# Performance work log

Measured on AMD Instinct MI355X. Metric: run time of the kernel, lower is better.

Reference implementation:

```python
import jax, jax.numpy as jnp
import numpy as np

E = 8        # moe_num_experts
TOPK = 2     # moe_topk
H = 1024     # hidden_size
I = 1024     # intermediate_size
ISH = I * 2  # shared experts intermediate (intermediate_size * moe_num_shared_experts)
B, S = 2, 1024


def setup_inputs() -> dict:
    key = jax.random.key(0)
    ks = jax.random.split(key, 7)
    s = 0.02
    return {
        "hidden_states": jax.random.normal(ks[0], (B, S, H), jnp.float32),
        "w_router": jax.random.normal(ks[1], (H, E), jnp.float32) * s,
        "fc1_w": jax.random.normal(ks[2], (E, H, 2 * I), jnp.float32) * s,
        "fc2_w": jax.random.normal(ks[3], (E, I, H), jnp.float32) * s,
        "gate_w": jax.random.normal(ks[4], (H, ISH), jnp.float32) * s,
        "up_w": jax.random.normal(ks[5], (H, ISH), jnp.float32) * s,
        "down_w": jax.random.normal(ks[6], (ISH, H), jnp.float32) * s,
    }


def reference(hidden_states, w_router, fc1_w, fc2_w, gate_w, up_w, down_w):
    orig_shape = hidden_states.shape
    x = hidden_states.reshape(-1, orig_shape[-1])  # [N, H]

    # --- router: top-k + softmax over the top-k logits ---
    logits = x @ w_router                               # [N, E]
    top_logits, top_idx = jax.lax.top_k(logits, TOPK)   # [N, K]
    scores = jax.nn.softmax(top_logits, axis=-1)        # [N, K]

    # --- permute tokens so same-expert tokens are contiguous ---
    flat_idx = top_idx.reshape(-1)                      # [N*K]
    sorted_idx = jnp.argsort(flat_idx)                  # [N*K]
    permuted = x[sorted_idx // TOPK]                    # [N*K, H]
    eid = flat_idx[sorted_idx]                          # expert id per permuted slot

    # --- grouped expert SwiGLU MLP (masked per-expert GEMMs; masked rows
    #     contribute exactly zero since silu(0)*0 = 0 and 0 @ W = 0) ---
    out_perm = jnp.zeros((permuted.shape[0], orig_shape[-1]), x.dtype)
    for e in range(E):
        m = (eid == e).astype(x.dtype)[:, None]         # [N*K, 1]
        h1 = (permuted * m) @ fc1_w[e]                  # [N*K, 2I]
        proj, gate = jnp.split(h1, 2, axis=-1)
        out_perm = out_perm + (jax.nn.silu(proj) * gate) @ fc2_w[e]

    # --- unpermute and combine with router scores ---
    unperm = jnp.zeros_like(out_perm).at[sorted_idx].set(out_perm)  # [N*K, H]
    moe_out = (unperm.reshape(-1, TOPK, orig_shape[-1]) * scores[:, :, None]).sum(axis=1)
    moe_out = moe_out.reshape(orig_shape)

    # --- shared experts (LlamaMLP, SwiGLU) ---
    shared = (jax.nn.silu(hidden_states @ gate_w) * (hidden_states @ up_w)) @ down_w
    return moe_out + shared
```

## Files before the change

### kernel.cpp

```cpp
#include <hip/hip_runtime.h>
#include <cstdint>


#define E_ 8
#define H_ 1024
#define I_ 1024
#define ISH_ 2048
#define NTOK 2048

typedef unsigned short u16;
using bf16x8 = __attribute__((ext_vector_type(8))) __bf16;
using f32x4  = __attribute__((ext_vector_type(4))) float;

__device__ __forceinline__ u16 f2bf(float f) {
  union { float f; unsigned u; } v; v.f = f;
  unsigned r = v.u + 0x7fffu + ((v.u >> 16) & 1u);
  return (u16)(r >> 16);
}
__device__ __forceinline__ float bf2f(u16 u) {
  union { unsigned u; float f; } v; v.u = ((unsigned)u) << 16; return v.f;
}
__device__ __forceinline__ unsigned pk2(float lo, float hi) {
  return ((unsigned)f2bf(hi) << 16) | (unsigned)f2bf(lo);
}

typedef __attribute__((address_space(1))) const void glb_v;
typedef __attribute__((address_space(3))) void lds_v;
__device__ __forceinline__ void gl16(const void* g, void* l) {
  __builtin_amdgcn_global_load_lds((glb_v*)g, (lds_v*)l, 16, 0, 0);
}

__device__ __forceinline__ void router_body(const float* __restrict__ x,
                                            const float* __restrict__ wr,
                                            float* __restrict__ scores,
                                            int* __restrict__ cnt,
                                            int* __restrict__ list, int tk) {
  int lane = threadIdx.x & 63;
  const float* xr = x + (size_t)tk * H_;
  float acc[E_];
#pragma unroll
  for (int e = 0; e < E_; ++e) acc[e] = 0.f;
  int h0 = lane * 16;
#pragma unroll 4
  for (int i = 0; i < 16; ++i) {
    float xv = xr[h0 + i];
    const float* w = wr + (size_t)(h0 + i) * E_;
#pragma unroll
    for (int e = 0; e < E_; ++e) acc[e] = fmaf(xv, w[e], acc[e]);
  }
#pragma unroll
  for (int off = 32; off > 0; off >>= 1) {
#pragma unroll
    for (int e = 0; e < E_; ++e) acc[e] += __shfl_xor(acc[e], off, 64);
  }
  if (lane == 0) {
    int e0 = 0; float m0 = acc[0];
#pragma unroll
    for (int e = 1; e < E_; ++e) if (acc[e] > m0) { m0 = acc[e]; e0 = e; }
    int e1 = -1; float m1 = -1e30f;
#pragma unroll
    for (int e = 0; e < E_; ++e) if (e != e0 && acc[e] > m1) { m1 = acc[e]; e1 = e; }
    float s0 = 1.f / (1.f + __expf(m1 - m0));
    scores[tk * 2 + 0] = s0;
    scores[tk * 2 + 1] = 1.f - s0;
    int p0 = atomicAdd(&cnt[e0], 1); list[e0 * NTOK + p0] = tk * 2;
    int p1 = atomicAdd(&cnt[e1], 1); list[e1 * NTOK + p1] = tk * 2 + 1;
  }
}

__device__ __forceinline__ void wtrans(const float* __restrict__ src,
                                       u16* __restrict__ dst, int K, int N,
                                       int k0, int n0, void* smem) {
  unsigned* lt = (unsigned*)smem;
  int t = threadIdx.x;
  int c = t & 31, kb = t >> 5;
  const float* sp = src + (size_t)(k0 + kb * 8) * N + n0 + (c << 2);
  float v[8][4];
#pragma unroll
  for (int j2 = 0; j2 < 8; ++j2) {
    float4 f = *(const float4*)(sp + (size_t)j2 * N);
    v[j2][0] = f.x; v[j2][1] = f.y; v[j2][2] = f.z; v[j2][3] = f.w;
  }
#pragma unroll
  for (int j = 0; j < 4; ++j) {
    int nl = (c << 2) + j;
    uint4 o = make_uint4(pk2(v[0][j], v[1][j]), pk2(v[2][j], v[3][j]),
                         pk2(v[4][j], v[5][j]), pk2(v[6][j], v[7][j]));
    *(uint4*)&lt[nl * 32 + ((kb ^ (c & 7)) << 2)] = o;
  }
  __syncthreads();
#pragma unroll
  for (int it = 0; it < 4; ++it) {
    int lin = it * 256 + t;
    int nl = lin >> 3, kq = lin & 7;
    uint4 o = *(const uint4*)&lt[nl * 32 + ((kq ^ ((nl >> 2) & 7)) << 2)];
    *(uint4*)(dst + (size_t)(n0 + nl) * K + k0 + kq * 8) = o;
  }
}


__global__ __launch_bounds__(256) void prep_k(
    const float* __restrict__ x, const float* __restrict__ wr,
    float* __restrict__ scores, int* __restrict__ cnt, int* __restrict__ list,
    u16* __restrict__ xb,
    const float* __restrict__ fc1, const float* __restrict__ fc2,
    const float* __restrict__ gw, const float* __restrict__ uw,
    const float* __restrict__ dw,
    u16* __restrict__ fc1T, u16* __restrict__ fc2T, u16* __restrict__ gwT,
    u16* __restrict__ uwT, u16* __restrict__ dwT) {
  __shared__ __align__(16) char psm[16384];
  int bid = blockIdx.x, t = threadIdx.x;
  if (bid < 512) {
    router_body(x, wr, scores, cnt, list, bid * 4 + (t >> 6));
    return;
  }
  if (bid < 1024) {
    const float4* srcx = (const float4*)x;
    ushort4* dstx = (ushort4*)xb;
    int base = (bid - 512) * 1024 + t;
#pragma unroll
    for (int it = 0; it < 4; ++it) {
      float4 v = srcx[base + it * 256];
      ushort4 o;
      o.x = f2bf(v.x); o.y = f2bf(v.y); o.z = f2bf(v.z); o.w = f2bf(v.w);
      dstx[base + it * 256] = o;
    }
    return;
  }
  if (bid < 3072) {
    int b = bid - 1024;
    int e = b >> 8, q = b & 255;
    wtrans(fc1 + ((size_t)e << 21), fc1T + ((size_t)e << 21), 1024, 2048,
           (q & 15) * 64, (q >> 4) * 128, psm);
  } else if (bid < 3328) {
    int q = bid - 3072;
    wtrans(gw, gwT, 1024, 2048, (q & 15) * 64, (q >> 4) * 128, psm);
  } else if (bid < 3584) {
    int q = bid - 3328;
    wtrans(uw, uwT, 1024, 2048, (q & 15) * 64, (q >> 4) * 128, psm);
  } else if (bid < 4608) {
    int b = bid - 3584;
    int e = b >> 7, q = b & 127;
    wtrans(fc2 + ((size_t)e << 20), fc2T + ((size_t)e << 20), 1024, 1024,
           (q & 15) * 64, (q >> 4) * 128, psm);
  } else {
    int q = bid - 4608;
    wtrans(dw, dwT, 2048, 1024, (q & 31) * 64, (q >> 5) * 128, psm);
  }
}

__global__ __launch_bounds__(256, 2) void swiglu_f_k(
    const u16* __restrict__ xb, const int* __restrict__ cnt,
    const int* __restrict__ list, const u16* __restrict__ fc1T,
    const u16* __restrict__ gwT, const u16* __restrict__ uwT,
    u16* __restrict__ act, u16* __restrict__ tmp) {
  __shared__ __align__(16) u16 As[2][128][32];
  __shared__ __align__(16) u16 B1s[2][128][32];
  __shared__ __align__(16) u16 B2s[2][128][32];

  int bid = blockIdx.x;
  int m0, n0, Me, obase = 0, ldo;
  const u16 *B1, *B2;
  const int* rowmap = nullptr;
  u16* Out;
  if (bid < 256) {
    int mb = bid >> 4, nb = bid & 15;
    m0 = mb * 128; n0 = nb * 128; Me = NTOK;
    B1 = gwT + (size_t)n0 * 1024; B2 = uwT + (size_t)n0 * 1024;
    Out = tmp; ldo = ISH_;
  } else {
    int b2 = bid - 256; int e = b2 >> 7, r = b2 & 127, mb = r >> 3, nb = r & 7;
    Me = cnt[e]; m0 = mb * 128;
    if (m0 >= Me) return;
    n0 = nb * 128;
    rowmap = list + e * NTOK;
    const u16* fe = fc1T + ((size_t)e << 21);
    B1 = fe + (size_t)n0 * 1024;
    B2 = fe + (size_t)(1024 + n0) * 1024;
    int off = 0;
    for (int q = 0; q < e; ++q) off += cnt[q];
    obase = off;
    Out = act; ldo = I_;
  }
  int t = threadIdx.x, wid = t >> 6, lane = t & 63;
  int wm = wid & 1, wn = wid >> 1, lr = lane & 15, lkg = lane >> 4;
  int cq = lane & 3, crw = lane >> 2;

  const u16 *arow[2], *b1row[2], *b2row[2];
#pragma unroll
  for (int i = 0; i < 2; ++i) {
    int c = wid * 2 + i;
    int rl = m0 + c * 16 + crw;
    int rc = rl < Me ? rl : (Me - 1);
    int tok = rowmap ? (rowmap[rc] >> 1) : rc;
    arow[i] = xb + (size_t)tok * 1024 + cq * 8;
    int rb = c * 16 + crw;
    b1row[i] = B1 + (size_t)rb * 1024 + cq * 8;
    b2row[i] = B2 + (size_t)rb * 1024 + cq * 8;
  }

  auto stage = [&](int cb, int kk) {
#pragma unroll
    for (int i = 0; i < 2; ++i) {
      int c = wid * 2 + i;
      gl16(arow[i] + kk, (u16*)As + cb * 4096 + c * 512);
      gl16(b1row[i] + kk, (u16*)B1s + cb * 4096 + c * 512);
      gl16(b2row[i] + kk, (u16*)B2s + cb * 4096 + c * 512);
    }
  };

  f32x4 aP[4][4] = {}, aG[4][4] = {};
  auto compute = [&](int cb) {
    bf16x8 af[4];
#pragma unroll
    for (int f = 0; f < 4; ++f)
      af[f] = *(const bf16x8*)((u16*)As + cb * 4096 + (wm * 64 + f * 16 + lr) * 32 + lkg * 8);
#pragma unroll
    for (int fn = 0; fn < 4; ++fn) {
      bf16x8 b1 = *(const bf16x8*)((u16*)B1s + cb * 4096 + (wn * 64 + fn * 16 + lr) * 32 + lkg * 8);
      bf16x8 b2 = *(const bf16x8*)((u16*)B2s + cb * 4096 + (wn * 64 + fn * 16 + lr) * 32 + lkg * 8);
#pragma unroll
      for (int fm = 0; fm < 4; ++fm) {
        aP[fm][fn] = __builtin_amdgcn_mfma_f32_16x16x32_bf16(af[fm], b1, aP[fm][fn], 0, 0, 0);
        aG[fm][fn] = __builtin_amdgcn_mfma_f32_16x16x32_bf16(af[fm], b2, aG[fm][fn], 0, 0, 0);
      }
    }
  };

  stage(0, 0);
  __syncthreads();
  int cur = 0;
  for (int k0 = 32; k0 < 1024; k0 += 32) {
    stage(cur ^ 1, k0);
    compute(cur);
    __syncthreads();
    cur ^= 1;
  }
  compute(cur);

#pragma unroll
  for (int fm = 0; fm < 4; ++fm)
#pragma unroll
    for (int fn = 0; fn < 4; ++fn)
#pragma unroll
      for (int j = 0; j < 4; ++j) {
        int row = m0 + wm * 64 + fm * 16 + lkg * 4 + j;
        if (row < Me) {
          float p = aP[fm][fn][j], g = aG[fm][fn][j];
          float s = p / (1.f + __expf(-p)) * g;
          Out[(size_t)(obase + row) * ldo + n0 + wn * 64 + fn * 16 + lr] = f2bf(s);
        }
      }
}

template <int MODE>
__device__ __forceinline__ void out_body(
    const u16* __restrict__ Ab, const u16* __restrict__ Bb, int Me, int m0,
    int n0, const int* __restrict__ listE, const float* __restrict__ scores,
    float* __restrict__ out, char* smem) {
  constexpr int BNx = MODE ? 64 : 128;
  constexpr int FN = BNx / 32;
  constexpr int KROW = MODE ? 2048 : 1024;
  constexpr int BCH = BNx / 64;
  u16* As = (u16*)smem;
  u16* Bs = (u16*)(smem + 16384);

  int t = threadIdx.x, wid = t >> 6, lane = t & 63;
  int wm = wid & 1, wn = wid >> 1, lr = lane & 15, lkg = lane >> 4;
  int cq = lane & 3, crw = lane >> 2;

  const u16* arow[2];
#pragma unroll
  for (int i = 0; i < 2; ++i) {
    int c = wid * 2 + i;
    int rl = m0 + c * 16 + crw;
    int rc = rl < Me ? rl : (Me - 1);
    arow[i] = Ab + (size_t)rc * KROW + cq * 8;
  }
  const u16* brow[BCH];
#pragma unroll
  for (int i = 0; i < BCH; ++i) {
    int c = wid * BCH + i;
    brow[i] = Bb + (size_t)(c * 16 + crw) * KROW + cq * 8;
  }

  auto stage = [&](int cb, int kk) {
#pragma unroll
    for (int i = 0; i < 2; ++i)
      gl16(arow[i] + kk, As + cb * 4096 + (wid * 2 + i) * 512);
#pragma unroll
    for (int i = 0; i < BCH; ++i)
      gl16(brow[i] + kk, Bs + cb * (BNx * 32) + (wid * BCH + i) * 512);
  };

  f32x4 acc[4][FN] = {};
  auto compute = [&](int cb) {
    bf16x8 af[4];
#pragma unroll
    for (int f = 0; f < 4; ++f)
      af[f] = *(const bf16x8*)(As + cb * 4096 + (wm * 64 + f * 16 + lr) * 32 + lkg * 8);
#pragma unroll
    for (int fn = 0; fn < FN; ++fn) {
      bf16x8 bb = *(const bf16x8*)(Bs + cb * (BNx * 32) +
                                   (wn * (BNx / 2) + fn * 16 + lr) * 32 + lkg * 8);
#pragma unroll
      for (int fm = 0; fm < 4; ++fm)
        acc[fm][fn] = __builtin_amdgcn_mfma_f32_16x16x32_bf16(af[fm], bb, acc[fm][fn], 0, 0, 0);
    }
  };

  stage(0, 0);
  __syncthreads();
  int cur = 0;
  for (int k0 = 32; k0 < 1024; k0 += 32) {
    stage(cur ^ 1, k0);
    compute(cur);
    __syncthreads();
    cur ^= 1;
  }
  compute(cur);

#pragma unroll
  for (int fm = 0; fm < 4; ++fm)
#pragma unroll
    for (int fn = 0; fn < FN; ++fn)
#pragma unroll
      for (int j = 0; j < 4; ++j) {
        int row = m0 + wm * 64 + fm * 16 + lkg * 4 + j;
        if (row < Me) {
          float v = acc[fm][fn][j];
          int c = n0 + wn * (BNx / 2) + fn * 16 + lr;
          if (MODE == 0) {
            int slot = listE[row];
            atomicAdd(&out[(size_t)(slot >> 1) * H_ + c], v * scores[slot]);
          } else {
            atomicAdd(&out[(size_t)row * H_ + c], v);
          }
        }
      }
}

__global__ __launch_bounds__(256, 2) void out_f_k(
    const u16* __restrict__ act, const u16* __restrict__ fc2T,
    const u16* __restrict__ tmp, const u16* __restrict__ dwT,
    const int* __restrict__ cnt, const int* __restrict__ list,
    const float* __restrict__ scores, float* __restrict__ out) {
  __shared__ __align__(16) char smem[32768];
  int bid = blockIdx.x;
  if (bid < 1024) {
    int e = bid >> 7, r = bid & 127, mb = r >> 3, nb = r & 7;
    int Me = cnt[e], m0 = mb * 128;
    if (m0 >= Me) return;
    int off = 0;
    for (int q = 0; q < e; ++q) off += cnt[q];
    out_body<0>(act + (size_t)off * 1024,
                fc2T + ((size_t)e << 20) + (size_t)(nb * 128) * 1024,
                Me, m0, nb * 128, list + e * NTOK, scores, out, smem);
  } else {
    int r = bid - 1024, ks = r >> 8, rr = r & 255, mb = rr >> 4, nb = rr & 15;
    out_body<1>(tmp + ks * 1024,
                dwT + (size_t)(nb * 64) * 2048 + ks * 1024,
                NTOK, mb * 128, nb * 64, nullptr, nullptr, out, smem);
  }
}

#define BM 128
#define BN 64
#define BK 32
#define PK (BK + 8)

__global__ void router_k(const float* __restrict__ x, const float* __restrict__ wr,
                         float* __restrict__ scores, int* __restrict__ cnt,
                         int* __restrict__ list) {
  int wid = threadIdx.x >> 6;
  int tk = blockIdx.x * 4 + wid;
  if (tk >= NTOK) return;
  router_body(x, wr, scores, cnt, list, tk);
}

__global__ void offs_k(const int* __restrict__ cnt, int* __restrict__ offs) {
  if (threadIdx.x == 0 && blockIdx.x == 0) {
    int s = 0;
    for (int e = 0; e < E_; ++e) { offs[e] = s; s += cnt[e]; }
  }
}

__global__ void cvt_k(const float* __restrict__ x, u16* __restrict__ xb, int n4) {
  int i = blockIdx.x * blockDim.x + threadIdx.x;
  if (i >= n4) return;
  float4 v = reinterpret_cast<const float4*>(x)[i];
  ushort4 o;
  o.x = f2bf(v.x); o.y = f2bf(v.y); o.z = f2bf(v.z); o.w = f2bf(v.w);
  reinterpret_cast<ushort4*>(xb)[i] = o;
}

template <int EXPERT>
__global__ __launch_bounds__(256) void swiglu_gemm_k(
    const u16* __restrict__ A, int lda,
    const int* __restrict__ list, const int* __restrict__ cnt, const int* __restrict__ offs,
    const float* __restrict__ B1g, const float* __restrict__ B2g, int ldb, long long bstride,
    u16* __restrict__ Out, int ldo, int K) {
  __shared__ u16 As[BM][PK];
  __shared__ u16 Bs[2][BN][PK];
  int e = EXPERT ? blockIdx.z : 0;
  int Me = EXPERT ? cnt[e] : NTOK;
  int m0 = blockIdx.y * BM;
  if (m0 >= Me) return;
  int n0 = blockIdx.x * BN;
  const int* rowmap = EXPERT ? (list + e * NTOK) : nullptr;
  const float* B1 = B1g + (EXPERT ? (long long)e * bstride : 0);
  const float* B2 = B2g + (EXPERT ? (long long)e * bstride : 0);
  int t = threadIdx.x, wid = t >> 6, lane = t & 63;
  int wm = wid & 1, wn = wid >> 1, lr = lane & 15, lkg = lane >> 4;
  f32x4 accP[4][2] = {}, accG[4][2] = {};
  for (int k0 = 0; k0 < K; k0 += BK) {
#pragma unroll
// ... 85 lines not shown
      float4 f = *reinterpret_cast<const float4*>(B + (size_t)(k0 + kr) * ldb + n0 + c);
      Bs[c + 0][kr] = f2bf(f.x); Bs[c + 1][kr] = f2bf(f.y);
      Bs[c + 2][kr] = f2bf(f.z); Bs[c + 3][kr] = f2bf(f.w);
    }
    __syncthreads();
    bf16x8 af[4];
#pragma unroll
    for (int fm = 0; fm < 4; ++fm)
      af[fm] = *reinterpret_cast<const bf16x8*>(&As[wm * 64 + fm * 16 + lr][lkg * 8]);
#pragma unroll
    for (int fn = 0; fn < 2; ++fn) {
      bf16x8 bb = *reinterpret_cast<const bf16x8*>(&Bs[wn * 32 + fn * 16 + lr][lkg * 8]);
#pragma unroll
      for (int fm = 0; fm < 4; ++fm)
        acc[fm][fn] = __builtin_amdgcn_mfma_f32_16x16x32_bf16(af[fm], bb, acc[fm][fn], 0, 0, 0);
    }
    __syncthreads();
  }
#pragma unroll
  for (int fm = 0; fm < 4; ++fm)
#pragma unroll
    for (int fn = 0; fn < 2; ++fn)
#pragma unroll
      for (int j = 0; j < 4; ++j) {
        int grow = wm * 64 + fm * 16 + lkg * 4 + j, gcol = wn * 32 + fn * 16 + lr;
        int row = m0 + grow;
        if (row < Me) {
          float v = acc[fm][fn][j];
          int c = n0 + gcol;
          if (EXPERT) {
            int slot = list[e * NTOK + row];
            Out[(size_t)slot * H_ + c] = v * scores[slot];
          } else {
            Out[(size_t)row * H_ + c] =
                v + outbuf[(size_t)(2 * row) * H_ + c] + outbuf[(size_t)(2 * row + 1) * H_ + c];
          }
        }
      }
}

extern "C" void kernel_launch(void* const* d_in, const int* in_sizes, int n_in,
                              void* d_out, int out_size, void* d_ws, size_t ws_size,
                              hipStream_t stream) {
  const float* x   = (const float*)d_in[0];
  const float* wr  = (const float*)d_in[1];
  const float* fc1 = (const float*)d_in[2];
  const float* fc2 = (const float*)d_in[3];
  const float* gw  = (const float*)d_in[4];
  const float* uw  = (const float*)d_in[5];
  const float* dw  = (const float*)d_in[6];
  float* out = (float*)d_out;
  char* ws = (char*)d_ws;

  const size_t NEED_FAST = 131072ull + (88ull << 20);
  if (ws_size >= NEED_FAST) {
    float* scores = (float*)ws;
    int* cnt  = (int*)(ws + 16384);
    int* list = (int*)(ws + 16512);
    u16* xb   = (u16*)(ws + 131072);
    u16* act  = (u16*)(ws + 131072 + (4ll << 20));
    u16* tmp  = (u16*)(ws + 131072 + (12ll << 20));
    u16* fc1T = (u16*)(ws + 131072 + (28ll << 20));
    u16* fc2T = (u16*)(ws + 131072 + (60ll << 20));
    u16* gwT  = (u16*)(ws + 131072 + (76ll << 20));
    u16* uwT  = (u16*)(ws + 131072 + (80ll << 20));
    u16* dwT  = (u16*)(ws + 131072 + (84ll << 20));

    hipMemsetAsync(cnt, 0, 128, stream);
    hipMemsetAsync(out, 0, (size_t)NTOK * H_ * sizeof(float), stream);
    prep_k<<<4864, 256, 0, stream>>>(x, wr, scores, cnt, list, xb,
                                     fc1, fc2, gw, uw, dw,
                                     fc1T, fc2T, gwT, uwT, dwT);
    swiglu_f_k<<<1280, 256, 0, stream>>>(xb, cnt, list, fc1T, gwT, uwT, act, tmp);
    out_f_k<<<1536, 256, 0, stream>>>(act, fc2T, tmp, dwT, cnt, list, scores, out);
  } else {
    float* scores = (float*)(ws);
    int*   cnt    = (int*)(ws + (16 << 10));
    int*   offs   = (int*)(ws + (16 << 10) + 128);
    int*   list   = (int*)(ws + (16 << 10) + 256);
    u16*   xb     = (u16*)(ws + (96 << 10));
    u16*   act    = (u16*)(ws + (96 << 10) + (4ll << 20));
    u16*   tmp    = (u16*)(ws + (96 << 10) + (12ll << 20));
    float* outbuf = (float*)(ws + (96 << 10) + (20ll << 20));

    hipMemsetAsync(cnt, 0, E_ * sizeof(int), stream);
    router_k<<<NTOK / 4, 256, 0, stream>>>(x, wr, scores, cnt, list);
    offs_k<<<1, 64, 0, stream>>>(cnt, offs);
    cvt_k<<<(NTOK * H_ / 4 + 255) / 256, 256, 0, stream>>>(x, xb, NTOK * H_ / 4);
    swiglu_gemm_k<1><<<dim3(I_ / BN, NTOK / BM, E_), 256, 0, stream>>>(
        xb, H_, list, cnt, offs, fc1, fc1 + I_, 2 * I_, (long long)H_ * 2 * I_, act, I_, H_);
    out_gemm_k<1><<<dim3(H_ / BN, NTOK / BM, E_), 256, 0, stream>>>(
        act, I_, cnt, offs, list, scores, fc2, H_, (long long)I_ * H_, outbuf, nullptr, I_);
    swiglu_gemm_k<0><<<dim3(ISH_ / BN, NTOK / BM, 1), 256, 0, stream>>>(
        xb, H_, nullptr, nullptr, nullptr, gw, uw, ISH_, 0, tmp, ISH_, H_);
    out_gemm_k<0><<<dim3(H_ / BN, NTOK / BM, 1), 256, 0, stream>>>(
        tmp, ISH_, nullptr, nullptr, nullptr, nullptr, dw, H_, 0, out, outbuf, ISH_);
  }
  (void)in_sizes; (void)n_in; (void)out_size;
}
```

Measured before the change: 254.4 us.

## Fuse fp32 weight conversion into GEMM B-tile loads, drop transpose prep pass

Removes the separate prep pass that transposed and converted all expert and shared weights to bf16 in workspace. The GEMM kernels now read fp32 weights directly in row-major layout and convert and transpose them into swizzled LDS tiles through registers, while activations keep the async global-to-LDS path. This avoids writing and rereading about 88MB of converted weights. In exchange, each weight tile is converted again by every M-block that uses it, the fp32 reads are twice as large, and B is single-buffered with an extra barrier per k-step.

```diff
diff --git a/kernel.cpp b/kernel.cpp
--- a/kernel.cpp
+++ b/kernel.cpp
@@ -17,9 +17,6 @@
   unsigned r = v.u + 0x7fffu + ((v.u >> 16) & 1u);
   return (u16)(r >> 16);
 }
-__device__ __forceinline__ float bf2f(u16 u) {
-  union { unsigned u; float f; } v; v.u = ((unsigned)u) << 16; return v.f;
-}
 __device__ __forceinline__ unsigned pk2(float lo, float hi) {
   return ((unsigned)f2bf(hi) << 16) | (unsigned)f2bf(lo);
 }
@@ -28,6 +25,14 @@
 typedef __attribute__((address_space(3))) void lds_v;
 __device__ __forceinline__ void gl16(const void* g, void* l) {
   __builtin_amdgcn_global_load_lds((glb_v*)g, (lds_v*)l, 16, 0, 0);
+}
+
+__device__ __forceinline__ bf16x8 rdfrag(const u16* base, int row, int lkg) {
+  int off = row * 64 + 16 * (lkg ^ ((row >> 2) & 3));
+  return *reinterpret_cast<const bf16x8*>(reinterpret_cast<const char*>(base) + off);
+}
+__device__ __forceinline__ f32x4 mfma16(bf16x8 a, bf16x8 b, f32x4 c) {
+  return __builtin_amdgcn_mfma_f32_16x16x32_bf16(a, b, c, 0, 0, 0);
 }
 
 __device__ __forceinline__ void router_body(const float* __restrict__ x,
@@ -68,105 +73,47 @@
   }
 }
 
-__device__ __forceinline__ void wtrans(const float* __restrict__ src,
-                                       u16* __restrict__ dst, int K, int N,
-                                       int k0, int n0, void* smem) {
-  unsigned* lt = (unsigned*)smem;
-  int t = threadIdx.x;
-  int c = t & 31, kb = t >> 5;
-  const float* sp = src + (size_t)(k0 + kb * 8) * N + n0 + (c << 2);
-  float v[8][4];
-#pragma unroll
-  for (int j2 = 0; j2 < 8; ++j2) {
-    float4 f = *(const float4*)(sp + (size_t)j2 * N);
-    v[j2][0] = f.x; v[j2][1] = f.y; v[j2][2] = f.z; v[j2][3] = f.w;
-  }
-#pragma unroll
-  for (int j = 0; j < 4; ++j) {
-    int nl = (c << 2) + j;
-    uint4 o = make_uint4(pk2(v[0][j], v[1][j]), pk2(v[2][j], v[3][j]),
-                         pk2(v[4][j], v[5][j]), pk2(v[6][j], v[7][j]));
-    *(uint4*)&lt[nl * 32 + ((kb ^ (c & 7)) << 2)] = o;
-  }
-  __syncthreads();
-#pragma unroll
-  for (int it = 0; it < 4; ++it) {
-    int lin = it * 256 + t;
-    int nl = lin >> 3, kq = lin & 7;
-    uint4 o = *(const uint4*)&lt[nl * 32 + ((kq ^ ((nl >> 2) & 7)) << 2)];
-    *(uint4*)(dst + (size_t)(n0 + nl) * K + k0 + kq * 8) = o;
-  }
-}
-
-
-__global__ __launch_bounds__(256) void prep_k(
+
+__global__ __launch_bounds__(256) void rc_k(
     const float* __restrict__ x, const float* __restrict__ wr,
     float* __restrict__ scores, int* __restrict__ cnt, int* __restrict__ list,
-    u16* __restrict__ xb,
-    const float* __restrict__ fc1, const float* __restrict__ fc2,
-    const float* __restrict__ gw, const float* __restrict__ uw,
-    const float* __restrict__ dw,
-    u16* __restrict__ fc1T, u16* __restrict__ fc2T, u16* __restrict__ gwT,
-    u16* __restrict__ uwT, u16* __restrict__ dwT) {
-  __shared__ __align__(16) char psm[16384];
+    u16* __restrict__ xb) {
   int bid = blockIdx.x, t = threadIdx.x;
   if (bid < 512) {
     router_body(x, wr, scores, cnt, list, bid * 4 + (t >> 6));
     return;
   }
-  if (bid < 1024) {
-    const float4* srcx = (const float4*)x;
-    ushort4* dstx = (ushort4*)xb;
-    int base = (bid - 512) * 1024 + t;
-#pragma unroll
-    for (int it = 0; it < 4; ++it) {
-      float4 v = srcx[base + it * 256];
-      ushort4 o;
-      o.x = f2bf(v.x); o.y = f2bf(v.y); o.z = f2bf(v.z); o.w = f2bf(v.w);
-      dstx[base + it * 256] = o;
-    }
-    return;
-  }
-  if (bid < 3072) {
-    int b = bid - 1024;
-    int e = b >> 8, q = b & 255;
-    wtrans(fc1 + ((size_t)e << 21), fc1T + ((size_t)e << 21), 1024, 2048,
-           (q & 15) * 64, (q >> 4) * 128, psm);
-  } else if (bid < 3328) {
-    int q = bid - 3072;
-    wtrans(gw, gwT, 1024, 2048, (q & 15) * 64, (q >> 4) * 128, psm);
-  } else if (bid < 3584) {
-    int q = bid - 3328;
-    wtrans(uw, uwT, 1024, 2048, (q & 15) * 64, (q >> 4) * 128, psm);
-  } else if (bid < 4608) {
-    int b = bid - 3584;
-    int e = b >> 7, q = b & 127;
-    wtrans(fc2 + ((size_t)e << 20), fc2T + ((size_t)e << 20), 1024, 1024,
-           (q & 15) * 64, (q >> 4) * 128, psm);
-  } else {
-    int q = bid - 4608;
-    wtrans(dw, dwT, 2048, 1024, (q & 31) * 64, (q >> 5) * 128, psm);
-  }
-}
-
-__global__ __launch_bounds__(256, 2) void swiglu_f_k(
+  const float4* srcx = (const float4*)x;
+  ushort4* dstx = (ushort4*)xb;
+  int base = (bid - 512) * 1024 + t;
+#pragma unroll
+  for (int it = 0; it < 4; ++it) {
+    float4 v = srcx[base + it * 256];
+    ushort4 o;
+    o.x = f2bf(v.x); o.y = f2bf(v.y); o.z = f2bf(v.z); o.w = f2bf(v.w);
+    dstx[base + it * 256] = o;
+  }
+}
+
+__global__ __launch_bounds__(256, 2) void swiglu2_k(
     const u16* __restrict__ xb, const int* __restrict__ cnt,
-    const int* __restrict__ list, const u16* __restrict__ fc1T,
-    const u16* __restrict__ gwT, const u16* __restrict__ uwT,
+    const int* __restrict__ list,
+    const float* __restrict__ fc1, const float* __restrict__ gw,
+    const float* __restrict__ uw,
     u16* __restrict__ act, u16* __restrict__ tmp) {
   __shared__ __align__(16) u16 As[2][128][32];
-  __shared__ __align__(16) u16 B1s[2][128][32];
-  __shared__ __align__(16) u16 B2s[2][128][32];
+  __shared__ __align__(16) u16 B1s[128][32];
+  __shared__ __align__(16) u16 B2s[128][32];
 
   int bid = blockIdx.x;
   int m0, n0, Me, obase = 0, ldo;
-  const u16 *B1, *B2;
+  const float *B1, *B2;
   const int* rowmap = nullptr;
   u16* Out;
   if (bid < 256) {
     int mb = bid >> 4, nb = bid & 15;
     m0 = mb * 128; n0 = nb * 128; Me = NTOK;
-    B1 = gwT + (size_t)n0 * 1024; B2 = uwT + (size_t)n0 * 1024;
+    B1 = gw + n0; B2 = uw + n0;
     Out = tmp; ldo = ISH_;
   } else {
     int b2 = bid - 256; int e = b2 >> 7, r = b2 & 127, mb = r >> 3, nb = r & 7;
@@ -174,69 +121,98 @@
     if (m0 >= Me) return;
     n0 = nb * 128;
     rowmap = list + e * NTOK;
-    const u16* fe = fc1T + ((size_t)e << 21);
-    B1 = fe + (size_t)n0 * 1024;
-    B2 = fe + (size_t)(1024 + n0) * 1024;
+    const float* fe = fc1 + ((size_t)e << 21);
+    B1 = fe + n0; B2 = fe + 1024 + n0;
     int off = 0;
     for (int q = 0; q < e; ++q) off += cnt[q];
-    obase = off;
-    Out = act; ldo = I_;
-  }
+    obase = off; Out = act; ldo = I_;
+  }
+  const int ldb = 2048;
   int t = threadIdx.x, wid = t >> 6, lane = t & 63;
   int wm = wid & 1, wn = wid >> 1, lr = lane & 15, lkg = lane >> 4;
-  int cq = lane & 3, crw = lane >> 2;
-
-  const u16 *arow[2], *b1row[2], *b2row[2];
+  int crw = lane >> 2;
+  int cqs = (lane & 3) ^ ((lane >> 4) & 3);
+
+  const u16* arow[2];
 #pragma unroll
   for (int i = 0; i < 2; ++i) {
     int c = wid * 2 + i;
     int rl = m0 + c * 16 + crw;
     int rc = rl < Me ? rl : (Me - 1);
     int tok = rowmap ? (rowmap[rc] >> 1) : rc;
-    arow[i] = xb + (size_t)tok * 1024 + cq * 8;
-    int rb = c * 16 + crw;
-    b1row[i] = B1 + (size_t)rb * 1024 + cq * 8;
-    b2row[i] = B2 + (size_t)rb * 1024 + cq * 8;
-  }
-
-  auto stage = [&](int cb, int kk) {
-#pragma unroll
-    for (int i = 0; i < 2; ++i) {
-      int c = wid * 2 + i;
-      gl16(arow[i] + kk, (u16*)As + cb * 4096 + c * 512);
-      gl16(b1row[i] + kk, (u16*)B1s + cb * 4096 + c * 512);
-      gl16(b2row[i] + kk, (u16*)B2s + cb * 4096 + c * 512);
-    }
+    arow[i] = xb + (size_t)tok * 1024 + cqs * 8;
+  }
+  int bn4 = (t & 31) * 4;
+  int bkq = (t >> 5) * 4;
+  int q8 = t >> 5;
+  int wboff[4];
+#pragma unroll
+  for (int j = 0; j < 4; ++j) {
+    int n = bn4 + j;
+    wboff[j] = n * 64 + 16 * ((q8 >> 1) ^ ((n >> 2) & 3)) + 8 * (q8 & 1);
+  }
+
+  float4 bv1[4], bv2[4];
+  auto loadB = [&](int k0) {
+    const float* p1 = B1 + (size_t)(k0 + bkq) * ldb + bn4;
+    const float* p2 = B2 + (size_t)(k0 + bkq) * ldb + bn4;
+#pragma unroll
+    for (int i = 0; i < 4; ++i) {
+      bv1[i] = *reinterpret_cast<const float4*>(p1 + (size_t)i * ldb);
+      bv2[i] = *reinterpret_cast<const float4*>(p2 + (size_t)i * ldb);
+    }
+  };
+  auto writeB = [&]() {
+#pragma unroll
+    for (int j = 0; j < 4; ++j) {
+      unsigned lo1 = pk2(((const float*)&bv1[0])[j], ((const float*)&bv1[1])[j]);
+      unsigned hi1 = pk2(((const float*)&bv1[2])[j], ((const float*)&bv1[3])[j]);
+      *reinterpret_cast<uint2*>(reinterpret_cast<char*>(&B1s[0][0]) + wboff[j]) =
+          make_uint2(lo1, hi1);
+      unsigned lo2 = pk2(((const float*)&bv2[0])[j], ((const float*)&bv2[1])[j]);
+      unsigned hi2 = pk2(((const float*)&bv2[2])[j], ((const float*)&bv2[3])[j]);
+      *reinterpret_cast<uint2*>(reinterpret_cast<char*>(&B2s[0][0]) + wboff[j]) =
+          make_uint2(lo2, hi2);
+    }
+  };
+  auto stageA = [&](int cb, int k0) {
+#pragma unroll
+    for (int i = 0; i < 2; ++i)
+      gl16(arow[i] + k0, (u16*)As + cb * 4096 + (wid * 2 + i) * 512);
   };
 
   f32x4 aP[4][4] = {}, aG[4][4] = {};
   auto compute = [&](int cb) {
+    const u16* Ab = (const u16*)As + cb * 4096;
     bf16x8 af[4];
 #pragma unroll
-    for (int f = 0; f < 4; ++f)
-      af[f] = *(const bf16x8*)((u16*)As + cb * 4096 + (wm * 64 + f * 16 + lr) * 32 + lkg * 8);
+    for (int f = 0; f < 4; ++f) af[f] = rdfrag(Ab, wm * 64 + f * 16 + lr, lkg);
 #pragma unroll
     for (int fn = 0; fn < 4; ++fn) {
-      bf16x8 b1 = *(const bf16x8*)((u16*)B1s + cb * 4096 + (wn * 64 + fn * 16 + lr) * 32 + lkg * 8);
-      bf16x8 b2 = *(const bf16x8*)((u16*)B2s + cb * 4096 + (wn * 64 + fn * 16 + lr) * 32 + lkg * 8);
+      bf16x8 b1 = rdfrag(&B1s[0][0], wn * 64 + fn * 16 + lr, lkg);
+      bf16x8 b2 = rdfrag(&B2s[0][0], wn * 64 + fn * 16 + lr, lkg);
 #pragma unroll
       for (int fm = 0; fm < 4; ++fm) {
-        aP[fm][fn] = __builtin_amdgcn_mfma_f32_16x16x32_bf16(af[fm], b1, aP[fm][fn], 0, 0, 0);
-        aG[fm][fn] = __builtin_amdgcn_mfma_f32_16x16x32_bf16(af[fm], b2, aG[fm][fn], 0, 0, 0);
-      }
-    }
-  };
-
-  stage(0, 0);
+        aP[fm][fn] = mfma16(af[fm], b1, aP[fm][fn]);
+        aG[fm][fn] = mfma16(af[fm], b2, aG[fm][fn]);
+      }
+    }
+  };
+
+  loadB(0);
+  stageA(0, 0);
+  writeB();
   __syncthreads();
   int cur = 0;
-  for (int k0 = 32; k0 < 1024; k0 += 32) {
-    stage(cur ^ 1, k0);
+  for (int k0 = 0; k0 < 1024; k0 += 32) {
+    bool more = (k0 + 32) < 1024;
+    if (more) { stageA(cur ^ 1, k0 + 32); loadB(k0 + 32); }
     compute(cur);
     __syncthreads();
+    if (more) writeB();
+    __syncthreads();
     cur ^= 1;
   }
-  compute(cur);
 
 #pragma unroll
   for (int fm = 0; fm < 4; ++fm)
@@ -244,7 +220,7 @@
     for (int fn = 0; fn < 4; ++fn)
 #pragma unroll
       for (int j = 0; j < 4; ++j) {
-        int row = m0 + wm * 64 + fm * 16 + lkg * 4 + j;
+        int row = m0 + wm * 64 + fm * 16 + (lane >> 4) * 4 + j;
         if (row < Me) {
           float p = aP[fm][fn][j], g = aG[fm][fn][j];
           float s = p / (1.f + __expf(-p)) * g;
@@ -254,20 +230,20 @@
 }
 
 template <int MODE>
-__device__ __forceinline__ void out_body(
-    const u16* __restrict__ Ab, const u16* __restrict__ Bb, int Me, int m0,
-    int n0, const int* __restrict__ listE, const float* __restrict__ scores,
-    float* __restrict__ out, char* smem) {
+__device__ __forceinline__ void out_body2(
+    const u16* __restrict__ Ab, int lda, const float* __restrict__ Bb,
+    int Me, int m0, int n0, const int* __restrict__ listE,
+    const float* __restrict__ scores, float* __restrict__ out, char* smem) {
   constexpr int BNx = MODE ? 64 : 128;
   constexpr int FN = BNx / 32;
-  constexpr int KROW = MODE ? 2048 : 1024;
-  constexpr int BCH = BNx / 64;
   u16* As = (u16*)smem;
   u16* Bs = (u16*)(smem + 16384);
+  const int ldb = 1024;
 
   int t = threadIdx.x, wid = t >> 6, lane = t & 63;
   int wm = wid & 1, wn = wid >> 1, lr = lane & 15, lkg = lane >> 4;
-  int cq = lane & 3, crw = lane >> 2;
+  int crw = lane >> 2;
+  int cqs = (lane & 3) ^ ((lane >> 4) & 3);
 
   const u16* arow[2];
 #pragma unroll
@@ -275,50 +251,84 @@
     int c = wid * 2 + i;
     int rl = m0 + c * 16 + crw;
     int rc = rl < Me ? rl : (Me - 1);
-    arow[i] = Ab + (size_t)rc * KROW + cq * 8;
-  }
-  const u16* brow[BCH];
-#pragma unroll
-  for (int i = 0; i < BCH; ++i) {
-    int c = wid * BCH + i;
-    brow[i] = Bb + (size_t)(c * 16 + crw) * KROW + cq * 8;
-  }
-
-  auto stage = [&](int cb, int kk) {
+    arow[i] = Ab + (size_t)rc * lda + cqs * 8;
+  }
+
+  int bn4, bkq, wboff[4];
+  if (MODE == 0) {
+    bn4 = (t & 31) * 4; bkq = (t >> 5) * 4;
+    int q8 = t >> 5;
+#pragma unroll
+    for (int j = 0; j < 4; ++j) {
+      int n = bn4 + j;
+      wboff[j] = n * 64 + 16 * ((q8 >> 1) ^ ((n >> 2) & 3)) + 8 * (q8 & 1);
+    }
+  } else {
+    bn4 = (t & 15) * 4; bkq = (t >> 4) * 2;
+    int p = t >> 4;
+#pragma unroll
+    for (int j = 0; j < 4; ++j) {
+      int n = bn4 + j;
+      wboff[j] = n * 64 + 16 * ((p >> 2) ^ ((n >> 2) & 3)) + 4 * (p & 3);
+    }
+  }
+
+  float4 bv[4];
+  auto loadB = [&](int k0) {
+    const float* p = Bb + (size_t)(k0 + bkq) * ldb + bn4;
+#pragma unroll
+    for (int i = 0; i < (MODE ? 2 : 4); ++i)
+      bv[i] = *reinterpret_cast<const float4*>(p + (size_t)i * ldb);
+  };
+  auto writeB = [&]() {
+#pragma unroll
+    for (int j = 0; j < 4; ++j) {
+      if (MODE == 0) {
+        unsigned lo = pk2(((const float*)&bv[0])[j], ((const float*)&bv[1])[j]);
+        unsigned hi = pk2(((const float*)&bv[2])[j], ((const float*)&bv[3])[j]);
+        *reinterpret_cast<uint2*>(reinterpret_cast<char*>(Bs) + wboff[j]) =
+            make_uint2(lo, hi);
+      } else {
+        unsigned w = pk2(((const float*)&bv[0])[j], ((const float*)&bv[1])[j]);
+        *reinterpret_cast<unsigned*>(reinterpret_cast<char*>(Bs) + wboff[j]) = w;
+      }
+    }
+  };
+  auto stageA = [&](int cb, int k0) {
 #pragma unroll
     for (int i = 0; i < 2; ++i)
-      gl16(arow[i] + kk, As + cb * 4096 + (wid * 2 + i) * 512);
-#pragma unroll
-    for (int i = 0; i < BCH; ++i)
-      gl16(brow[i] + kk, Bs + cb * (BNx * 32) + (wid * BCH + i) * 512);
+      gl16(arow[i] + k0, As + cb * 4096 + (wid * 2 + i) * 512);
   };
 
   f32x4 acc[4][FN] = {};
   auto compute = [&](int cb) {
+    const u16* Ap = As + cb * 4096;
     bf16x8 af[4];
 #pragma unroll
-    for (int f = 0; f < 4; ++f)
-      af[f] = *(const bf16x8*)(As + cb * 4096 + (wm * 64 + f * 16 + lr) * 32 + lkg * 8);
+    for (int f = 0; f < 4; ++f) af[f] = rdfrag(Ap, wm * 64 + f * 16 + lr, lkg);
 #pragma unroll
     for (int fn = 0; fn < FN; ++fn) {
-      bf16x8 bb = *(const bf16x8*)(Bs + cb * (BNx * 32) +
-                                   (wn * (BNx / 2) + fn * 16 + lr) * 32 + lkg * 8);
+      bf16x8 bb = rdfrag(Bs, wn * (BNx / 2) + fn * 16 + lr, lkg);
 #pragma unroll
       for (int fm = 0; fm < 4; ++fm)
-        acc[fm][fn] = __builtin_amdgcn_mfma_f32_16x16x32_bf16(af[fm], bb, acc[fm][fn], 0, 0, 0);
-    }
-  };
-
-  stage(0, 0);
+        acc[fm][fn] = mfma16(af[fm], bb, acc[fm][fn]);
+    }
+  };
+
+  loadB(0);
+  stageA(0, 0);
+  writeB();
   __syncthreads();
   int cur = 0;
-  for (int k0 = 32; k0 < 1024; k0 += 32) {
-    stage(cur ^ 1, k0);
+  for (int k0 = 0; k0 < 1024; k0 += 32) {
+    bool more = (k0 + 32) < 1024;
+    if (more) { stageA(cur ^ 1, k0 + 32); loadB(k0 + 32); }
     compute(cur);
     __syncthreads();
+    if (more) writeB();
+    __syncthreads();
     cur ^= 1;
   }
-  compute(cur);
 
 #pragma unroll
   for (int fm = 0; fm < 4; ++fm)
@@ -340,12 +350,12 @@
       }
 }
 
-__global__ __launch_bounds__(256, 2) void out_f_k(
-    const u16* __restrict__ act, const u16* __restrict__ fc2T,
-    const u16* __restrict__ tmp, const u16* __restrict__ dwT,
+__global__ __launch_bounds__(256, 2) void out2_k(
+    const u16* __restrict__ act, const float* __restrict__ fc2,
+    const u16* __restrict__ tmp, const float* __restrict__ dw,
     const int* __restrict__ cnt, const int* __restrict__ list,
     const float* __restrict__ scores, float* __restrict__ out) {
-  __shared__ __align__(16) char smem[32768];
+  __shared__ __align__(16) char smem[24576];
   int bid = blockIdx.x;
   if (bid < 1024) {
     int e = bid >> 7, r = bid & 127, mb = r >> 3, nb = r & 7;
@@ -353,14 +363,14 @@
     if (m0 >= Me) return;
     int off = 0;
     for (int q = 0; q < e; ++q) off += cnt[q];
-    out_body<0>(act + (size_t)off * 1024,
-                fc2T + ((size_t)e << 20) + (size_t)(nb * 128) * 1024,
-                Me, m0, nb * 128, list + e * NTOK, scores, out, smem);
+    out_body2<0>(act + (size_t)off * 1024, 1024,
+                 fc2 + ((size_t)e << 20) + (nb * 128),
+                 Me, m0, nb * 128, list + e * NTOK, scores, out, smem);
   } else {
     int r = bid - 1024, ks = r >> 8, rr = r & 255, mb = rr >> 4, nb = rr & 15;
-    out_body<1>(tmp + ks * 1024,
-                dwT + (size_t)(nb * 64) * 2048 + ks * 1024,
-                NTOK, mb * 128, nb * 64, nullptr, nullptr, out, smem);
+    out_body2<1>(tmp + ks * 1024, 2048,
+                 dw + (size_t)ks * 1024 * 1024 + (nb * 64),
+                 NTOK, mb * 128, nb * 64, nullptr, nullptr, out, smem);
   }
 }
 
@@ -553,7 +563,7 @@
   float* out = (float*)d_out;
   char* ws = (char*)d_ws;
 
-  const size_t NEED_FAST = 131072ull + (88ull << 20);
+  const size_t NEED_FAST = 131072ull + (20ull << 20);
   if (ws_size >= NEED_FAST) {
     float* scores = (float*)ws;
     int* cnt  = (int*)(ws + 16384);
@@ -561,19 +571,12 @@
     u16* xb   = (u16*)(ws + 131072);
     u16* act  = (u16*)(ws + 131072 + (4ll << 20));
     u16* tmp  = (u16*)(ws + 131072 + (12ll << 20));
-    u16* fc1T = (u16*)(ws + 131072 + (28ll << 20));
-    u16* fc2T = (u16*)(ws + 131072 + (60ll << 20));
-    u16* gwT  = (u16*)(ws + 131072 + (76ll << 20));
-    u16* uwT  = (u16*)(ws + 131072 + (80ll << 20));
-    u16* dwT  = (u16*)(ws + 131072 + (84ll << 20));
 
     hipMemsetAsync(cnt, 0, 128, stream);
     hipMemsetAsync(out, 0, (size_t)NTOK * H_ * sizeof(float), stream);
-    prep_k<<<4864, 256, 0, stream>>>(x, wr, scores, cnt, list, xb,
-                                     fc1, fc2, gw, uw, dw,
-                                     fc1T, fc2T, gwT, uwT, dwT);
-    swiglu_f_k<<<1280, 256, 0, stream>>>(xb, cnt, list, fc1T, gwT, uwT, act, tmp);
-    out_f_k<<<1536, 256, 0, stream>>>(act, fc2T, tmp, dwT, cnt, list, scores, out);
+    rc_k<<<1024, 256, 0, stream>>>(x, wr, scores, cnt, list, xb);
+    swiglu2_k<<<1280, 256, 0, stream>>>(xb, cnt, list, fc1, gw, uw, act, tmp);
+    out2_k<<<1536, 256, 0, stream>>>(act, fc2, tmp, dw, cnt, list, scores, out);
   } else {
     float* scores = (float*)(ws);
     int*   cnt    = (int*)(ws + (16 << 10));
```

Result: slower. 267.4 us (+5.1%).

## Store transposed weights pre-tiled so GEMM B tiles load contiguously

Applied to the files above, without the earlier changes.

The weight transpose now writes bf16 weights in 128x32 tile-contiguous blocks, so each GEMM stage loads its B tile as one contiguous 8 KB chunk instead of 128 strided row segments. The shared-expert down projection in the output kernel also moves from 128x64 tiles to 128x128 tiles, cutting that part from 512 to 256 blocks and giving one uniform kernel body. The aim is better coalescing and less address arithmetic on B loads, plus less A-tile refetching for the down projection. The cost is a non-standard weight layout tied to these tile sizes, and fewer blocks for the shared down projection.

```diff
diff --git a/kernel.cpp b/kernel.cpp
--- a/kernel.cpp
+++ b/kernel.cpp
@@ -17,9 +17,6 @@
   unsigned r = v.u + 0x7fffu + ((v.u >> 16) & 1u);
   return (u16)(r >> 16);
 }
-__device__ __forceinline__ float bf2f(u16 u) {
-  union { unsigned u; float f; } v; v.u = ((unsigned)u) << 16; return v.f;
-}
 __device__ __forceinline__ unsigned pk2(float lo, float hi) {
   return ((unsigned)f2bf(hi) << 16) | (unsigned)f2bf(lo);
 }
@@ -28,6 +25,9 @@
 typedef __attribute__((address_space(3))) void lds_v;
 __device__ __forceinline__ void gl16(const void* g, void* l) {
   __builtin_amdgcn_global_load_lds((glb_v*)g, (lds_v*)l, 16, 0, 0);
+}
+__device__ __forceinline__ f32x4 mfma16(bf16x8 a, bf16x8 b, f32x4 c) {
+  return __builtin_amdgcn_mfma_f32_16x16x32_bf16(a, b, c, 0, 0, 0);
 }
 
 __device__ __forceinline__ void router_body(const float* __restrict__ x,
@@ -68,13 +68,14 @@
   }
 }
 
-__device__ __forceinline__ void wtrans(const float* __restrict__ src,
-                                       u16* __restrict__ dst, int K, int N,
-                                       int k0, int n0, void* smem) {
+__device__ __forceinline__ void wtrans2(const float* __restrict__ src,
+                                        u16* __restrict__ dst, int K, int N,
+                                        int kb, int nb, void* smem) {
   unsigned* lt = (unsigned*)smem;
   int t = threadIdx.x;
-  int c = t & 31, kb = t >> 5;
-  const float* sp = src + (size_t)(k0 + kb * 8) * N + n0 + (c << 2);
+  int c = t & 31, k8 = t >> 5;
+  int k0 = kb * 64, n0 = nb * 128;
+  const float* sp = src + (size_t)(k0 + k8 * 8) * N + n0 + (c << 2);
   float v[8][4];
 #pragma unroll
   for (int j2 = 0; j2 < 8; ++j2) {
@@ -86,20 +87,22 @@
     int nl = (c << 2) + j;
     uint4 o = make_uint4(pk2(v[0][j], v[1][j]), pk2(v[2][j], v[3][j]),
                          pk2(v[4][j], v[5][j]), pk2(v[6][j], v[7][j]));
-    *(uint4*)&lt[nl * 32 + ((kb ^ (c & 7)) << 2)] = o;
+    *(uint4*)&lt[nl * 32 + ((k8 ^ (c & 7)) << 2)] = o;
   }
   __syncthreads();
+  int ktiles = K >> 5;
+  u16* tb = dst + (size_t)(nb * ktiles + kb * 2) * 4096;
 #pragma unroll
   for (int it = 0; it < 4; ++it) {
     int lin = it * 256 + t;
     int nl = lin >> 3, kq = lin & 7;
     uint4 o = *(const uint4*)&lt[nl * 32 + ((kq ^ ((nl >> 2) & 7)) << 2)];
-    *(uint4*)(dst + (size_t)(n0 + nl) * K + k0 + kq * 8) = o;
-  }
-}
-
-
-__global__ __launch_bounds__(256) void prep_k(
+    *(uint4*)(tb + (kq >> 2) * 4096 + nl * 32 + (kq & 3) * 8) = o;
+  }
+}
+
+
+__global__ __launch_bounds__(256) void prep2_k(
     const float* __restrict__ x, const float* __restrict__ wr,
     float* __restrict__ scores, int* __restrict__ cnt, int* __restrict__ list,
     u16* __restrict__ xb,
@@ -130,33 +133,33 @@
   if (bid < 3072) {
     int b = bid - 1024;
     int e = b >> 8, q = b & 255;
-    wtrans(fc1 + ((size_t)e << 21), fc1T + ((size_t)e << 21), 1024, 2048,
-           (q & 15) * 64, (q >> 4) * 128, psm);
+    wtrans2(fc1 + ((size_t)e << 21), fc1T + ((size_t)e << 21), 1024, 2048,
+            q & 15, q >> 4, psm);
   } else if (bid < 3328) {
     int q = bid - 3072;
-    wtrans(gw, gwT, 1024, 2048, (q & 15) * 64, (q >> 4) * 128, psm);
+    wtrans2(gw, gwT, 1024, 2048, q & 15, q >> 4, psm);
   } else if (bid < 3584) {
     int q = bid - 3328;
-    wtrans(uw, uwT, 1024, 2048, (q & 15) * 64, (q >> 4) * 128, psm);
+    wtrans2(uw, uwT, 1024, 2048, q & 15, q >> 4, psm);
   } else if (bid < 4608) {
     int b = bid - 3584;
     int e = b >> 7, q = b & 127;
-    wtrans(fc2 + ((size_t)e << 20), fc2T + ((size_t)e << 20), 1024, 1024,
-           (q & 15) * 64, (q >> 4) * 128, psm);
+    wtrans2(fc2 + ((size_t)e << 20), fc2T + ((size_t)e << 20), 1024, 1024,
+            q & 15, q >> 4, psm);
   } else {
     int q = bid - 4608;
-    wtrans(dw, dwT, 2048, 1024, (q & 31) * 64, (q >> 5) * 128, psm);
-  }
-}
-
-__global__ __launch_bounds__(256, 2) void swiglu_f_k(
+    wtrans2(dw, dwT, 2048, 1024, q & 31, q >> 5, psm);
+  }
+}
+
+__global__ __launch_bounds__(256, 2) void swiglu3_k(
     const u16* __restrict__ xb, const int* __restrict__ cnt,
     const int* __restrict__ list, const u16* __restrict__ fc1T,
     const u16* __restrict__ gwT, const u16* __restrict__ uwT,
     u16* __restrict__ act, u16* __restrict__ tmp) {
-  __shared__ __align__(16) u16 As[2][128][32];
-  __shared__ __align__(16) u16 B1s[2][128][32];
-  __shared__ __align__(16) u16 B2s[2][128][32];
+  __shared__ __align__(16) u16 As[2][4096];
+  __shared__ __align__(16) u16 B1s[2][4096];
+  __shared__ __align__(16) u16 B2s[2][4096];
 
   int bid = blockIdx.x;
   int m0, n0, Me, obase = 0, ldo;
@@ -166,7 +169,8 @@
   if (bid < 256) {
     int mb = bid >> 4, nb = bid & 15;
     m0 = mb * 128; n0 = nb * 128; Me = NTOK;
-    B1 = gwT + (size_t)n0 * 1024; B2 = uwT + (size_t)n0 * 1024;
+    B1 = gwT + (size_t)(nb * 32) * 4096;
+    B2 = uwT + (size_t)(nb * 32) * 4096;
     Out = tmp; ldo = ISH_;
   } else {
     int b2 = bid - 256; int e = b2 >> 7, r = b2 & 127, mb = r >> 3, nb = r & 7;
@@ -175,18 +179,17 @@
     n0 = nb * 128;
     rowmap = list + e * NTOK;
     const u16* fe = fc1T + ((size_t)e << 21);
-    B1 = fe + (size_t)n0 * 1024;
-    B2 = fe + (size_t)(1024 + n0) * 1024;
+    B1 = fe + (size_t)(nb * 32) * 4096;
+    B2 = fe + (size_t)((8 + nb) * 32) * 4096;
     int off = 0;
     for (int q = 0; q < e; ++q) off += cnt[q];
-    obase = off;
-    Out = act; ldo = I_;
+    obase = off; Out = act; ldo = I_;
   }
   int t = threadIdx.x, wid = t >> 6, lane = t & 63;
   int wm = wid & 1, wn = wid >> 1, lr = lane & 15, lkg = lane >> 4;
   int cq = lane & 3, crw = lane >> 2;
 
-  const u16 *arow[2], *b1row[2], *b2row[2];
+  const u16* arow[2];
 #pragma unroll
   for (int i = 0; i < 2; ++i) {
     int c = wid * 2 + i;
@@ -194,18 +197,16 @@
     int rc = rl < Me ? rl : (Me - 1);
     int tok = rowmap ? (rowmap[rc] >> 1) : rc;
     arow[i] = xb + (size_t)tok * 1024 + cq * 8;
-    int rb = c * 16 + crw;
-    b1row[i] = B1 + (size_t)rb * 1024 + cq * 8;
-    b2row[i] = B2 + (size_t)rb * 1024 + cq * 8;
-  }
-
-  auto stage = [&](int cb, int kk) {
+  }
+
+  auto stage = [&](int cb, int kt) {
 #pragma unroll
     for (int i = 0; i < 2; ++i) {
       int c = wid * 2 + i;
-      gl16(arow[i] + kk, (u16*)As + cb * 4096 + c * 512);
-      gl16(b1row[i] + kk, (u16*)B1s + cb * 4096 + c * 512);
-      gl16(b2row[i] + kk, (u16*)B2s + cb * 4096 + c * 512);
+      int bo = wid * 1024 + i * 512;
+      gl16(arow[i] + kt * 32, As[cb] + c * 512);
+      gl16(B1 + kt * 4096 + bo + lane * 8, B1s[cb] + bo);
+      gl16(B2 + kt * 4096 + bo + lane * 8, B2s[cb] + bo);
     }
   };
 
@@ -214,15 +215,15 @@
     bf16x8 af[4];
 #pragma unroll
     for (int f = 0; f < 4; ++f)
-      af[f] = *(const bf16x8*)((u16*)As + cb * 4096 + (wm * 64 + f * 16 + lr) * 32 + lkg * 8);
+      af[f] = *(const bf16x8*)(As[cb] + (wm * 64 + f * 16 + lr) * 32 + lkg * 8);
 #pragma unroll
     for (int fn = 0; fn < 4; ++fn) {
-      bf16x8 b1 = *(const bf16x8*)((u16*)B1s + cb * 4096 + (wn * 64 + fn * 16 + lr) * 32 + lkg * 8);
-      bf16x8 b2 = *(const bf16x8*)((u16*)B2s + cb * 4096 + (wn * 64 + fn * 16 + lr) * 32 + lkg * 8);
+      bf16x8 b1 = *(const bf16x8*)(B1s[cb] + (wn * 64 + fn * 16 + lr) * 32 + lkg * 8);
+      bf16x8 b2 = *(const bf16x8*)(B2s[cb] + (wn * 64 + fn * 16 + lr) * 32 + lkg * 8);
 #pragma unroll
       for (int fm = 0; fm < 4; ++fm) {
-        aP[fm][fn] = __builtin_amdgcn_mfma_f32_16x16x32_bf16(af[fm], b1, aP[fm][fn], 0, 0, 0);
-        aG[fm][fn] = __builtin_amdgcn_mfma_f32_16x16x32_bf16(af[fm], b2, aG[fm][fn], 0, 0, 0);
+        aP[fm][fn] = mfma16(af[fm], b1, aP[fm][fn]);
+        aG[fm][fn] = mfma16(af[fm], b2, aG[fm][fn]);
       }
     }
   };
@@ -230,8 +231,8 @@
   stage(0, 0);
   __syncthreads();
   int cur = 0;
-  for (int k0 = 32; k0 < 1024; k0 += 32) {
-    stage(cur ^ 1, k0);
+  for (int kt = 1; kt < 32; ++kt) {
+    stage(cur ^ 1, kt);
     compute(cur);
     __syncthreads();
     cur ^= 1;
@@ -253,18 +254,35 @@
       }
 }
 
-template <int MODE>
-__device__ __forceinline__ void out_body(
-    const u16* __restrict__ Ab, const u16* __restrict__ Bb, int Me, int m0,
-    int n0, const int* __restrict__ listE, const float* __restrict__ scores,
-    float* __restrict__ out, char* smem) {
-  constexpr int BNx = MODE ? 64 : 128;
-  constexpr int FN = BNx / 32;
-  constexpr int KROW = MODE ? 2048 : 1024;
-  constexpr int BCH = BNx / 64;
-  u16* As = (u16*)smem;
-  u16* Bs = (u16*)(smem + 16384);
-
+__global__ __launch_bounds__(256, 2) void out3_k(
+    const u16* __restrict__ act, const u16* __restrict__ fc2T,
+    const u16* __restrict__ tmp, const u16* __restrict__ dwT,
+    const int* __restrict__ cnt, const int* __restrict__ list,
+    const float* __restrict__ scores, float* __restrict__ out) {
+  __shared__ __align__(16) u16 As[2][4096];
+  __shared__ __align__(16) u16 Bs[2][4096];
+
+  int bid = blockIdx.x;
+  int Me, m0, n0, lda, akoff = 0, mode, e = 0;
+  const u16 *Ab, *Bt;
+  const int* listE = nullptr;
+  if (bid < 1024) {
+    e = bid >> 7; int r = bid & 127, mb = r >> 3, nb = r & 7;
+    Me = cnt[e]; m0 = mb * 128;
+    if (m0 >= Me) return;
+    n0 = nb * 128;
+    int off = 0;
+    for (int q = 0; q < e; ++q) off += cnt[q];
+    Ab = act + (size_t)off * 1024; lda = 1024;
+    Bt = fc2T + ((size_t)e << 20) + (size_t)(nb * 32) * 4096;
+    listE = list + e * NTOK; mode = 0;
+  } else {
+    int r = bid - 1024, ks = r >> 7, rr = r & 127, mb = rr >> 3, nb = rr & 7;
+    Me = NTOK; m0 = mb * 128; n0 = nb * 128;
+    Ab = tmp; lda = 2048; akoff = ks * 1024;
+    Bt = dwT + (size_t)(nb * 64 + ks * 32) * 4096;
+    mode = 1;
+  }
   int t = threadIdx.x, wid = t >> 6, lane = t & 63;
   int wm = wid & 1, wn = wid >> 1, lr = lane & 15, lkg = lane >> 4;
   int cq = lane & 3, crw = lane >> 2;
@@ -275,45 +293,39 @@
     int c = wid * 2 + i;
     int rl = m0 + c * 16 + crw;
     int rc = rl < Me ? rl : (Me - 1);
-    arow[i] = Ab + (size_t)rc * KROW + cq * 8;
-  }
-  const u16* brow[BCH];
-#pragma unroll
-  for (int i = 0; i < BCH; ++i) {
-    int c = wid * BCH + i;
-    brow[i] = Bb + (size_t)(c * 16 + crw) * KROW + cq * 8;
-  }
-
-  auto stage = [&](int cb, int kk) {
-#pragma unroll
-    for (int i = 0; i < 2; ++i)
-      gl16(arow[i] + kk, As + cb * 4096 + (wid * 2 + i) * 512);
-#pragma unroll
-    for (int i = 0; i < BCH; ++i)
-      gl16(brow[i] + kk, Bs + cb * (BNx * 32) + (wid * BCH + i) * 512);
+    arow[i] = Ab + (size_t)rc * lda + akoff + cq * 8;
+  }
+
+  auto stage = [&](int cb, int kt) {
+#pragma unroll
+    for (int i = 0; i < 2; ++i) {
+      int c = wid * 2 + i;
+      int bo = wid * 1024 + i * 512;
+      gl16(arow[i] + kt * 32, As[cb] + c * 512);
+      gl16(Bt + kt * 4096 + bo + lane * 8, Bs[cb] + bo);
+    }
   };
 
-  f32x4 acc[4][FN] = {};
+  f32x4 acc[4][4] = {};
   auto compute = [&](int cb) {
     bf16x8 af[4];
 #pragma unroll
     for (int f = 0; f < 4; ++f)
-      af[f] = *(const bf16x8*)(As + cb * 4096 + (wm * 64 + f * 16 + lr) * 32 + lkg * 8);
-#pragma unroll
-    for (int fn = 0; fn < FN; ++fn) {
-      bf16x8 bb = *(const bf16x8*)(Bs + cb * (BNx * 32) +
-                                   (wn * (BNx / 2) + fn * 16 + lr) * 32 + lkg * 8);
+      af[f] = *(const bf16x8*)(As[cb] + (wm * 64 + f * 16 + lr) * 32 + lkg * 8);
+#pragma unroll
+    for (int fn = 0; fn < 4; ++fn) {
+      bf16x8 bb = *(const bf16x8*)(Bs[cb] + (wn * 64 + fn * 16 + lr) * 32 + lkg * 8);
 #pragma unroll
       for (int fm = 0; fm < 4; ++fm)
-        acc[fm][fn] = __builtin_amdgcn_mfma_f32_16x16x32_bf16(af[fm], bb, acc[fm][fn], 0, 0, 0);
+        acc[fm][fn] = mfma16(af[fm], bb, acc[fm][fn]);
     }
   };
 
   stage(0, 0);
   __syncthreads();
   int cur = 0;
-  for (int k0 = 32; k0 < 1024; k0 += 32) {
-    stage(cur ^ 1, k0);
+  for (int kt = 1; kt < 32; ++kt) {
+    stage(cur ^ 1, kt);
     compute(cur);
     __syncthreads();
     cur ^= 1;
@@ -323,14 +335,14 @@
 #pragma unroll
   for (int fm = 0; fm < 4; ++fm)
 #pragma unroll
-    for (int fn = 0; fn < FN; ++fn)
+    for (int fn = 0; fn < 4; ++fn)
 #pragma unroll
       for (int j = 0; j < 4; ++j) {
         int row = m0 + wm * 64 + fm * 16 + lkg * 4 + j;
         if (row < Me) {
           float v = acc[fm][fn][j];
-          int c = n0 + wn * (BNx / 2) + fn * 16 + lr;
-          if (MODE == 0) {
+          int c = n0 + wn * 64 + fn * 16 + lr;
+          if (mode == 0) {
             int slot = listE[row];
             atomicAdd(&out[(size_t)(slot >> 1) * H_ + c], v * scores[slot]);
           } else {
@@ -338,30 +350,6 @@
           }
         }
       }
-}
-
-__global__ __launch_bounds__(256, 2) void out_f_k(
-    const u16* __restrict__ act, const u16* __restrict__ fc2T,
-    const u16* __restrict__ tmp, const u16* __restrict__ dwT,
-    const int* __restrict__ cnt, const int* __restrict__ list,
-    const float* __restrict__ scores, float* __restrict__ out) {
-  __shared__ __align__(16) char smem[32768];
-  int bid = blockIdx.x;
-  if (bid < 1024) {
-    int e = bid >> 7, r = bid & 127, mb = r >> 3, nb = r & 7;
-    int Me = cnt[e], m0 = mb * 128;
-    if (m0 >= Me) return;
-    int off = 0;
-    for (int q = 0; q < e; ++q) off += cnt[q];
-    out_body<0>(act + (size_t)off * 1024,
-                fc2T + ((size_t)e << 20) + (size_t)(nb * 128) * 1024,
-                Me, m0, nb * 128, list + e * NTOK, scores, out, smem);
-  } else {
-    int r = bid - 1024, ks = r >> 8, rr = r & 255, mb = rr >> 4, nb = rr & 15;
-    out_body<1>(tmp + ks * 1024,
-                dwT + (size_t)(nb * 64) * 2048 + ks * 1024,
-                NTOK, mb * 128, nb * 64, nullptr, nullptr, out, smem);
-  }
 }
 
 #define BM 128
@@ -569,11 +557,11 @@
 
     hipMemsetAsync(cnt, 0, 128, stream);
     hipMemsetAsync(out, 0, (size_t)NTOK * H_ * sizeof(float), stream);
-    prep_k<<<4864, 256, 0, stream>>>(x, wr, scores, cnt, list, xb,
-                                     fc1, fc2, gw, uw, dw,
-                                     fc1T, fc2T, gwT, uwT, dwT);
-    swiglu_f_k<<<1280, 256, 0, stream>>>(xb, cnt, list, fc1T, gwT, uwT, act, tmp);
-    out_f_k<<<1536, 256, 0, stream>>>(act, fc2T, tmp, dwT, cnt, list, scores, out);
+    prep2_k<<<4864, 256, 0, stream>>>(x, wr, scores, cnt, list, xb,
+                                      fc1, fc2, gw, uw, dw,
+                                      fc1T, fc2T, gwT, uwT, dwT);
+    swiglu3_k<<<1280, 256, 0, stream>>>(xb, cnt, list, fc1T, gwT, uwT, act, tmp);
+    out3_k<<<1280, 256, 0, stream>>>(act, fc2T, tmp, dwT, cnt, list, scores, out);
   } else {
     float* scores = (float*)(ws);
     int*   cnt    = (int*)(ws + (16 << 10));
```

After: 267.2 us. 5.0% more time.
